# Performance work log

Hardware: AMD Instinct MI355X
Metric: run time of the kernel (lower is better)

Reference implementation:

```python
import jax, jax.numpy as jnp
import numpy as np

NUM_HEADS = 16
HEAD_DIM = 64  # hidden_size 1024 / 16 heads


def setup_inputs() -> dict:
    key = jax.random.key(0)
    ks = jax.random.split(key, 4)
    B, S, H = 2, 2048, 1024
    scale = 0.02
    return {
        "hidden_states": jax.random.normal(ks[0], (B, S, H), jnp.float32),
        "attention_mask": jnp.zeros((B, 1, 1, S), jnp.float32),  # additive mask
        "Wq": jax.random.normal(ks[1], (H, H), jnp.float32) * scale,
        "bq": jnp.zeros((H,), jnp.float32),
        "Wk": jax.random.normal(ks[2], (H, H), jnp.float32) * scale,
        "bk": jnp.zeros((H,), jnp.float32),
        "Wv": jax.random.normal(ks[3], (H, H), jnp.float32) * scale,
        "bv": jnp.zeros((H,), jnp.float32),
    }


def _split_heads(x):
    B, S, H = x.shape
    return x.reshape(B, S, NUM_HEADS, HEAD_DIM).transpose(0, 2, 1, 3)  # [B,h,S,dh]


def reference(hidden_states, attention_mask, Wq, bq, Wk, bk, Wv, bv):
    q = _split_heads(hidden_states @ Wq + bq)
    k = _split_heads(hidden_states @ Wk + bk)
    v = _split_heads(hidden_states @ Wv + bv)
    # scaled dot-product scores [B,h,S,S]
    scores = jnp.einsum("bhqd,bhkd->bhqk", q, k) / np.sqrt(HEAD_DIM).astype(np.float32)
    scores = scores + attention_mask  # additive mask, broadcast [B,1,1,S]
    probs = jax.nn.softmax(scores, axis=-1)  # dropout prob = 0.0
    ctx = jnp.einsum("bhqk,bhkd->bhqd", probs, v)
    B, h, S, dh = ctx.shape
    return ctx.transpose(0, 2, 1, 3).reshape(B, S, h * dh)  # [B,S,hidden]
```

## Files before the change

kernel.cpp:

```cpp
#include <hip/hip_runtime.h>
#include <hip/hip_bf16.h>


typedef __bf16 bf16x8 __attribute__((ext_vector_type(8)));
typedef __bf16 bf16x4 __attribute__((ext_vector_type(4)));
typedef float f32x4 __attribute__((ext_vector_type(4)));
typedef float f32x16 __attribute__((ext_vector_type(16)));
typedef int i32x4 __attribute__((ext_vector_type(4)));

static constexpr int H = 1024;
static constexpr int S = 2048;
static constexpr int NH = 16;
static constexpr int DH = 64;
static constexpr float L2E = 1.4426950408889634f;

#if __has_builtin(__builtin_amdgcn_exp2f)
#define EXP2F(x) __builtin_amdgcn_exp2f(x)
#else
#define EXP2F(x) __builtin_exp2f(x)
#endif

__device__ inline void gll16(const void* g, void* l) {
  __builtin_amdgcn_global_load_lds(
      (const __attribute__((address_space(1))) void*)g,
      (__attribute__((address_space(3))) void*)l, 16, 0, 0);
}

__device__ inline int pack2bf(float lo, float hi) {
  unsigned short a = __builtin_bit_cast(unsigned short, (__bf16)lo);
  unsigned short b = __builtin_bit_cast(unsigned short, (__bf16)hi);
  return (int)(((unsigned)b << 16) | (unsigned)a);
}

__device__ inline void plswap(int& a, int& b) {
  asm volatile("v_permlane32_swap_b32 %0, %1" : "+v"(a), "+v"(b));
}

__global__ __launch_bounds__(256) void convert_kernel(
    const float* __restrict__ X, const float* __restrict__ W0,
    const float* __restrict__ W1, const float* __restrict__ W2,
    __bf16* __restrict__ Xb, __bf16* __restrict__ Wt) {
  __shared__ float T[64][65];
  const int bid = blockIdx.x, tid = threadIdx.x;
  if (bid < 2048) {
    size_t i = ((size_t)bid * 256 + tid) * 8;
    float4 f0 = *(const float4*)(X + i);
    float4 f1 = *(const float4*)(X + i + 4);
    bf16x8 o;
    o[0] = (__bf16)f0.x; o[1] = (__bf16)f0.y; o[2] = (__bf16)f0.z; o[3] = (__bf16)f0.w;
    o[4] = (__bf16)f1.x; o[5] = (__bf16)f1.y; o[6] = (__bf16)f1.z; o[7] = (__bf16)f1.w;
    *(bf16x8*)(Xb + i) = o;
    return;
  }
  const int wid = bid - 2048;
  const int z = wid >> 8, t = wid & 255;
  const int k0 = (t >> 4) * 64, n0 = (t & 15) * 64;
  const float* W = z == 0 ? W0 : (z == 1 ? W1 : W2);
  __bf16* Wo = Wt + (size_t)z * H * H;
#pragma unroll
  for (int it = 0; it < 4; ++it) {
    int r = it * 16 + (tid >> 4), c = (tid & 15) * 4;
    *(float4*)&T[r][c] = *(const float4*)&W[(size_t)(k0 + r) * H + n0 + c];
  }
  __syncthreads();
#pragma unroll
  for (int it = 0; it < 4; ++it) {
    int n = it * 16 + (tid >> 4), c0 = (tid & 15) * 4;
    bf16x4 o;
#pragma unroll
    for (int j = 0; j < 4; ++j) o[j] = (__bf16)T[c0 + j][n];
    *(bf16x4*)&Wo[(size_t)(n0 + n) * H + k0 + c0] = o;
  }
}

__global__ __launch_bounds__(256, 3) void qkv_gemm_kernel(
    const __bf16* __restrict__ Xb, const __bf16* __restrict__ Wt,
    const float* __restrict__ bq, const float* __restrict__ bk,
    const float* __restrict__ bv,
    __bf16* __restrict__ Qt, __bf16* __restrict__ K, __bf16* __restrict__ Vt)
{
  __shared__ __bf16 As[128 * 64];
  __shared__ __bf16 Bs[128 * 64];

  const int tid = threadIdx.x, lane = tid & 63, w = tid >> 6;
  const int quad = lane >> 4, l16 = lane & 15;
  const int wsel = blockIdx.x >> 3;
  const int n0 = (blockIdx.x & 7) * 128;
  const int m0 = blockIdx.y * 128;
  const int wr = w & 1, wc = w >> 1;

  const __bf16* Wsel = Wt + (size_t)wsel * H * H;
  const float* bias = wsel == 0 ? bq : (wsel == 1 ? bk : bv);

  const __bf16* aptr[4];
  const __bf16* bptr[4];
#pragma unroll
  for (int i = 0; i < 4; ++i) {
    int s = w * 256 + i * 64 + lane;
    int row = s >> 3, col = s & 7, sc = col ^ (row & 7);
    aptr[i] = Xb + (size_t)(m0 + row) * H + sc * 8;
    bptr[i] = Wsel + (size_t)(n0 + row) * H + sc * 8;
  }

  f32x4 acc[4][4] = {};

  for (int k0 = 0; k0 < H; k0 += 64) {
    __syncthreads();
#pragma unroll
    for (int i = 0; i < 4; ++i) {
      gll16(aptr[i] + k0, &As[(w * 256 + i * 64) * 8]);
      gll16(bptr[i] + k0, &Bs[(w * 256 + i * 64) * 8]);
    }
    __syncthreads();
#pragma unroll
    for (int kc = 0; kc < 2; ++kc) {
      bf16x8 af[4], bfr[4];
#pragma unroll
      for (int t = 0; t < 4; ++t) {
        int ra = wr * 64 + t * 16 + l16;
        af[t] = *(const bf16x8*)&As[ra * 64 + (((kc * 4 + quad) ^ (ra & 7)) * 8)];
        int rb = wc * 64 + t * 16 + l16;
        bfr[t] = *(const bf16x8*)&Bs[rb * 64 + (((kc * 4 + quad) ^ (rb & 7)) * 8)];
      }
#pragma unroll
      for (int t = 0; t < 4; ++t)
#pragma unroll
        for (int u = 0; u < 4; ++u)
          acc[t][u] = __builtin_amdgcn_mfma_f32_16x16x32_bf16(af[t], bfr[u], acc[t][u], 0, 0, 0);
    }
  }

  const float qscale = 0.125f * L2E;
#pragma unroll
  for (int u = 0; u < 4; ++u) {
    int n = n0 + wc * 64 + u * 16 + l16;
    int head = n >> 6, d = n & 63;
    float bias_v = bias[n];
#pragma unroll
    for (int t = 0; t < 4; ++t) {
      int srow = m0 + wr * 64 + t * 16 + quad * 4;
      int b = srow >> 11, si = srow & (S - 1);
      int bh = b * NH + head;
      if (wsel == 1) {
        __bf16* dst = K + ((size_t)bh * S + si) * DH + d;
#pragma unroll
        for (int r = 0; r < 4; ++r)
          dst[(size_t)r * DH] = (__bf16)(acc[t][u][r] + bias_v);
      } else {
        float scl = wsel == 0 ? qscale : 1.0f;
        __bf16* outp = wsel == 0 ? Qt : Vt;
        bf16x4 o;
#pragma unroll
        for (int r = 0; r < 4; ++r) o[r] = (__bf16)((acc[t][u][r] + bias_v) * scl);
        *(bf16x4*)&outp[((size_t)bh * DH + d) * S + si] = o;
      }
    }
  }
}

__global__ __launch_bounds__(512, 4) void attn_kernel(
    const __bf16* __restrict__ Qt, const __bf16* __restrict__ K,
    const __bf16* __restrict__ Vt, const float* __restrict__ mask,
    float* __restrict__ out)
{
  __shared__ __bf16 Ks[2][2][64 * 64];
  __shared__ __bf16 Vs[2][2][64 * 64];
  __shared__ float  Ms[S];

  const int tid = threadIdx.x, lane = tid & 63, w = tid >> 6;
  const int l31 = lane & 31, hi = lane >> 5;
  const int wl = w & 3, wh = w >> 2;

  const int lin = blockIdx.y * 16 + blockIdx.x;
  const int v = (lin & 7) * 64 + (lin >> 3);
  const int bh = v >> 4, b = bh >> 4, h = bh & 15;
  const int q0 = (v & 15) * 128;

  const __bf16* Qb = Qt + (size_t)bh * DH * S;
  const __bf16* Kb = K + (size_t)bh * S * DH;
  const __bf16* Vb = Vt + (size_t)bh * DH * S;
  const float* mb = mask + (size_t)b * S;

  {
    int idx = tid * 4;
    float4 mv = *(const float4*)&mb[idx];
    float4 sv = {mv.x * L2E, mv.y * L2E, mv.z * L2E, mv.w * L2E};
    *(float4*)&Ms[idx] = sv;
  }

  const int q = q0 + wl * 32 + l31;
  bf16x8 qf[4];
#pragma unroll
  for (int kc = 0; kc < 4; ++kc)
#pragma unroll
    for (int j = 0; j < 8; ++j)
      qf[kc][j] = Qb[(size_t)(kc * 16 + hi * 8 + j) * S + q];

  const int kvbase = wh * 1024;
  const __bf16* kptr[2];
  const __bf16* vptr[2];
#pragma unroll
  for (int i = 0; i < 2; ++i) {
    int s = wl * 128 + i * 64 + lane;
    int row = s >> 3, col = s & 7, sc = col ^ (row & 7);
    kptr[i] = Kb + (size_t)(kvbase + row) * DH + sc * 8;
    vptr[i] = Vb + (size_t)row * S + kvbase + sc * 8;
  }

#pragma unroll
  for (int i = 0; i < 2; ++i) {
    gll16(kptr[i], &Ks[wh][0][(wl * 128 + i * 64 + lane) * 8]);
    gll16(vptr[i], &Vs[wh][0][(wl * 128 + i * 64 + lane) * 8]);
  }

  f32x16 o0 = {}, o1 = {};
  float dl = 0.0f;
  int cur = 0;

  for (int st = 0; st < 16; ++st) {
    __syncthreads();
    if (st + 1 < 16) {
      const int nxt = cur ^ 1;
#pragma unroll
      for (int i = 0; i < 2; ++i) {
        gll16(kptr[i] + (size_t)(st + 1) * 64 * DH, &Ks[wh][nxt][(wl * 128 + i * 64 + lane) * 8]);
        gll16(vptr[i] + (st + 1) * 64, &Vs[wh][nxt][(wl * 128 + i * 64 + lane) * 8]);
      }
    }
    const __bf16* Kc = &Ks[wh][cur][0];
    const __bf16* Vc = &Vs[wh][cur][0];
    const int kvabs = kvbase + st * 64;

#pragma unroll
    for (int kvsub = 0; kvsub < 2; ++kvsub) {
      const int rk = kvsub * 32 + l31;
      f32x16 cc;
#pragma unroll
      for (int g = 0; g < 4; ++g) {
        float4 m4 = *(const float4*)&Ms[kvabs + kvsub * 32 + g * 8 + hi * 4];
        cc[4 * g + 0] = m4.x; cc[4 * g + 1] = m4.y;
        cc[4 * g + 2] = m4.z; cc[4 * g + 3] = m4.w;
      }
      __builtin_amdgcn_s_setprio(1);
#pragma unroll
      for (int kc = 0; kc < 4; ++kc) {
        bf16x8 af = *(const bf16x8*)&Kc[rk * 64 + (((kc * 2 + hi) ^ (l31 & 7)) * 8)];
        cc = __builtin_amdgcn_mfma_f32_32x32x16_bf16(af, qf[kc], cc, 0, 0, 0);
      }
      __builtin_amdgcn_s_setprio(0);

      float p[16];
#pragma unroll
      for (int r = 0; r < 16; ++r) { p[r] = EXP2F(cc[r]); dl += p[r]; }
      int a0 = pack2bf(p[0],  p[1]),  b0 = pack2bf(p[2],  p[3]);
      int a1 = pack2bf(p[4],  p[5]),  b1 = pack2bf(p[6],  p[7]);
      int a2 = pack2bf(p[8],  p[9]),  b2 = pack2bf(p[10], p[11]);
      int a3 = pack2bf(p[12], p[13]), b3 = pack2bf(p[14], p[15]);
      plswap(a0, a1); plswap(b0, b1);
      plswap(a2, a3); plswap(b2, b3);
      i32x4 pi0 = {a0, b0, a1, b1};
      i32x4 pi1 = {a2, b2, a3, b3};
      bf16x8 pf0 = __builtin_bit_cast(bf16x8, pi0);
      bf16x8 pf1 = __builtin_bit_cast(bf16x8, pi1);

      __builtin_amdgcn_s_setprio(1);
#pragma unroll
      for (int pp = 0; pp < 2; ++pp) {
        const int pc = kvsub * 2 + pp;
        const bf16x8 pf = pp ? pf1 : pf0;
        bf16x8 vf0 = *(const bf16x8*)&Vc[l31 * 64 + (((pc * 2 + hi) ^ (l31 & 7)) * 8)];
        o0 = __builtin_amdgcn_mfma_f32_32x32x16_bf16(vf0, pf, o0, 0, 0, 0);
        bf16x8 vf1 = *(const bf16x8*)&Vc[(32 + l31) * 64 + (((pc * 2 + hi) ^ (l31 & 7)) * 8)];
        o1 = __builtin_amdgcn_mfma_f32_32x32x16_bf16(vf1, pf, o1, 0, 0, 0);
      }
      __builtin_amdgcn_s_setprio(0);
    }
    cur ^= 1;
  }

  float lsum = dl + __shfl_xor(dl, 32);

  __syncthreads();
  float* Os = (float*)&Ks[0][0][0];
  float* Ls = (float*)&Vs[0][0][0];
  if (wh == 1) {
#pragma unroll
    for (int g = 0; g < 4; ++g) {
      int s0 = (2 * g + hi) ^ (l31 & 7);
      float4 t0 = {o0[4 * g + 0], o0[4 * g + 1], o0[4 * g + 2], o0[4 * g + 3]};
      *(float4*)&Os[(wl * 32 + l31) * 64 + s0 * 4] = t0;
      int s1 = (8 + 2 * g + hi) ^ (l31 & 7);
      float4 t1 = {o1[4 * g + 0], o1[4 * g + 1], o1[4 * g + 2], o1[4 * g + 3]};
      *(float4*)&Os[(wl * 32 + l31) * 64 + s1 * 4] = t1;
    }
    if (hi == 0) Ls[wl * 32 + l31] = lsum;
  }
  __syncthreads();
  if (wh == 0) {
    float ltot = lsum + Ls[wl * 32 + l31];
    float invl = 1.0f / ltot;
#pragma unroll
    for (int g = 0; g < 4; ++g) {
      int d0 = g * 8 + hi * 4;
      int s0 = (2 * g + hi) ^ (l31 & 7);
      float4 u0 = *(const float4*)&Os[(wl * 32 + l31) * 64 + s0 * 4];
      float4 r0 = {(o0[4 * g + 0] + u0.x) * invl, (o0[4 * g + 1] + u0.y) * invl,
                   (o0[4 * g + 2] + u0.z) * invl, (o0[4 * g + 3] + u0.w) * invl};
      *(float4*)&out[((size_t)b * S + q) * H + h * DH + d0] = r0;
      int s1 = (8 + 2 * g + hi) ^ (l31 & 7);
      float4 u1 = *(const float4*)&Os[(wl * 32 + l31) * 64 + s1 * 4];
      float4 r1 = {(o1[4 * g + 0] + u1.x) * invl, (o1[4 * g + 1] + u1.y) * invl,
                   (o1[4 * g + 2] + u1.z) * invl, (o1[4 * g + 3] + u1.w) * invl};
      *(float4*)&out[((size_t)b * S + q) * H + h * DH + 32 + d0] = r1;
    }
  }
}

extern "C" void kernel_launch(void* const* d_in, const int* in_sizes, int n_in,
                              void* d_out, int out_size, void* d_ws, size_t ws_size,
                              hipStream_t stream) {
  const float* X    = (const float*)d_in[0];
  const float* mask = (const float*)d_in[1];
  const float* Wq   = (const float*)d_in[2];
  const float* bq   = (const float*)d_in[3];
  const float* Wk   = (const float*)d_in[4];
  const float* bk   = (const float*)d_in[5];
  const float* Wv   = (const float*)d_in[6];
  const float* bv   = (const float*)d_in[7];
  float* out = (float*)d_out;

  const size_t per = (size_t)2 * NH * S * DH;
  __bf16* Qws  = (__bf16*)d_ws;
  __bf16* Kws  = Qws + per;
  __bf16* Vtws = Kws + per;

  __bf16* Xb = (__bf16*)d_out;
  __bf16* Wt = Xb + per;

  convert_kernel<<<2816, 256, 0, stream>>>(X, Wq, Wk, Wv, Xb, Wt);
  qkv_gemm_kernel<<<dim3(24, 32), 256, 0, stream>>>(Xb, Wt, bq, bk, bv,
                                                    Qws, Kws, Vtws);
  attn_kernel<<<dim3(16, 32), 512, 0, stream>>>(Qws, Kws, Vtws, mask, out);
}
```

Baseline: 170.1 us.

## Single-buffer K/V tiles in shared memory to raise attention kernel occupancy

Replaces the double-buffered K/V shared-memory staging with a single flat buffer that is loaded and consumed each step, with two barriers per iteration. This shrinks the kernel's LDS footprint so more blocks can be resident per CU. The launch bound's minimum-blocks hint is raised from 4 to 8 to match. The trade-off is losing the prefetch overlap of the next tile with current compute, plus a tighter register budget that may cause spills.

```diff
diff --git a/kernel.cpp b/kernel.cpp
--- a/kernel.cpp
+++ b/kernel.cpp
@@ -158,14 +158,15 @@
   }
 }
 
-__global__ __launch_bounds__(512, 4) void attn_kernel(
+__global__ __launch_bounds__(512, 8) void attn_kernel(
     const __bf16* __restrict__ Qt, const __bf16* __restrict__ K,
     const __bf16* __restrict__ Vt, const float* __restrict__ mask,
     float* __restrict__ out)
 {
-  __shared__ __bf16 Ks[2][2][64 * 64];
-  __shared__ __bf16 Vs[2][2][64 * 64];
-  __shared__ float  Ms[S];
+  __shared__ __bf16 SM[20480];
+  __bf16* Ksb = SM;
+  __bf16* Vsb = SM + 8192;
+  float*  Ms  = (float*)(SM + 16384);
 
   const int tid = threadIdx.x, lane = tid & 63, w = tid >> 6;
   const int l31 = lane & 31, hi = lane >> 5;
@@ -207,28 +208,21 @@
     vptr[i] = Vb + (size_t)row * S + kvbase + sc * 8;
   }
 
-#pragma unroll
-  for (int i = 0; i < 2; ++i) {
-    gll16(kptr[i], &Ks[wh][0][(wl * 128 + i * 64 + lane) * 8]);
-    gll16(vptr[i], &Vs[wh][0][(wl * 128 + i * 64 + lane) * 8]);
-  }
-
   f32x16 o0 = {}, o1 = {};
   float dl = 0.0f;
-  int cur = 0;
 
   for (int st = 0; st < 16; ++st) {
     __syncthreads();
-    if (st + 1 < 16) {
-      const int nxt = cur ^ 1;
-#pragma unroll
-      for (int i = 0; i < 2; ++i) {
-        gll16(kptr[i] + (size_t)(st + 1) * 64 * DH, &Ks[wh][nxt][(wl * 128 + i * 64 + lane) * 8]);
-        gll16(vptr[i] + (st + 1) * 64, &Vs[wh][nxt][(wl * 128 + i * 64 + lane) * 8]);
-      }
-    }
-    const __bf16* Kc = &Ks[wh][cur][0];
-    const __bf16* Vc = &Vs[wh][cur][0];
+#pragma unroll
+    for (int i = 0; i < 2; ++i) {
+      gll16(kptr[i] + (size_t)st * 64 * DH,
+            &Ksb[wh * 4096 + (wl * 128 + i * 64 + lane) * 8]);
+      gll16(vptr[i] + st * 64,
+            &Vsb[wh * 4096 + (wl * 128 + i * 64 + lane) * 8]);
+    }
+    __syncthreads();
+    const __bf16* Kc = &Ksb[wh * 4096];
+    const __bf16* Vc = &Vsb[wh * 4096];
     const int kvabs = kvbase + st * 64;
 
 #pragma unroll
@@ -275,14 +269,13 @@
       }
       __builtin_amdgcn_s_setprio(0);
     }
-    cur ^= 1;
   }
 
   float lsum = dl + __shfl_xor(dl, 32);
 
   __syncthreads();
-  float* Os = (float*)&Ks[0][0][0];
-  float* Ls = (float*)&Vs[0][0][0];
+  float* Os = (float*)SM;
+  float* Ls = Ms;
   if (wh == 1) {
 #pragma unroll
     for (int g = 0; g < 4; ++g) {
```

New measurement: 248.7 us. 1.46x slower.
